# Kernel optimization log

Measured on AMD Instinct MI355X. Metric: run time of the kernel, lower is better.

The kernel has to match this reference:

```python
import jax, jax.numpy as jnp
import numpy as np
from jax import lax

C = 8          # bargs.channel
S = 1024       # bargs.test_sidelen
SIGMA = 1.0    # edge_sigma
KS = int(6 * SIGMA + 1)   # 7
PAD = KS // 2             # 3
BW = S // 6               # border_width
LAM, MU, TH = 5.0, 5.0, 1e-4


def _edge_kernel():
    coords = jnp.arange(KS, dtype=jnp.float32) - (KS - 1.0) / 2.0
    g1 = jnp.exp(-coords ** 2 / (2.0 * SIGMA ** 2))
    g1 = g1 / g1.sum()
    g2 = jnp.outer(g1, g1)
    return jnp.broadcast_to(g2, (C, 1, KS, KS))  # depthwise OIHW


def _alpha():
    # max applicable loop index among {row-dist, col-dist}; interior stays 1.
    r = jnp.arange(S)
    g = jnp.where(r < BW, r, jnp.where(S - 1 - r < BW, S - 1 - r, -1))  # [S]
    m = jnp.maximum(g[:, None], g[None, :])                              # [S,S]
    a = jnp.where(m >= 0, m.astype(jnp.float32) / BW, 1.0)
    return a[None, None]  # [1,1,S,S] broadcasts over channels


def _grad_spectrum():
    gv = jnp.array([[-1., -2., -1.], [0., 0., 0.], [1., 2., 1.]], jnp.float32)
    gh = gv.T
    gvf = jnp.fft.fft2(gv, s=(S, S))
    ghf = jnp.fft.fft2(gh, s=(S, S))
    return (jnp.abs(gvf) ** 2 + jnp.abs(ghf) ** 2).astype(jnp.float32)  # real


def _edge_blur(img, kernel, alpha):
    blurred = lax.conv_general_dilated(
        img, kernel, window_strides=(1, 1), padding=[(PAD, PAD), (PAD, PAD)],
        feature_group_count=C, dimension_numbers=('NCHW', 'OIHW', 'NCHW'))
    return alpha * img + (1.0 - alpha) * blurred


def setup_inputs() -> dict:
    key = jax.random.key(0)
    k1, k2 = jax.random.split(key)
    lms = jax.random.uniform(k1, (1, C, S, S), dtype=jnp.float32)
    fuse = jax.random.uniform(k2, (1, C, S, S), dtype=jnp.float32)
    return {"lms": lms, "fuse": fuse}


def reference(lms, fuse):
    kernel = _edge_kernel()
    alpha = _alpha()
    grad = _grad_spectrum()

    lms_fft = jnp.fft.fft2(_edge_blur(lms, kernel, alpha))
    fuse_fft = jnp.fft.fft2(_edge_blur(fuse, kernel, alpha))

    denom = jnp.abs(fuse_fft) ** 2 + LAM + MU * grad      # real [1,C,S,S]
    numer = jnp.conj(fuse_fft) * lms_fft
    psf = jnp.fft.fftshift(jnp.real(jnp.fft.ifft2(numer / denom)), axes=(-2, -1))
    psf = jnp.where(psf < TH, 0.0, psf)                   # [1,C,S,S]

    def crop(p):  # p: [S,S]
        row, col = jnp.unravel_index(jnp.argmax(p), p.shape)
        patch = lax.dynamic_slice(p, (row - 20, col - 20), (41, 41))
        return patch / jnp.sum(patch)

    psf_l = jax.vmap(crop)(psf[0])        # [C,41,41]
    return psf_l[:, None]                 # [C,1,41,41]
```

## Files before the change

kernel.cpp:

```cpp
#include <hip/hip_runtime.h>
#include <math.h>

#define SS 1024
#define NC 8
#define BWD 170
#define THRESH 1e-4f

typedef unsigned long long ull;

__device__ __forceinline__ float2 cmul(float2 a, float2 b) {
    return make_float2(a.x * b.x - a.y * b.y, a.x * b.y + a.y * b.x);
}

template <int DIRSIGN>
__device__ __forceinline__ void fft_fill_lut(float2* lut, int tid) {
    for (int i = tid; i < 768; i += 256) {
        float ang = (float)DIRSIGN * 6.28318530717958647692f * (float)i *
                    (1.0f / 1024.0f);
        float sv, cv;
        sincosf(ang, &sv, &cv);
        lut[i] = make_float2(cv, sv);
    }
}

template <int DIRSIGN, bool CONJ>
__device__ __forceinline__ void fft_stages(float2* bufA, float2* bufB,
                                           const float2* lut, int tid) {
    float2* src = bufA;
    float2* dst = bufB;
    #pragma unroll
    for (int t = 0; t < 5; ++t) {
        int s = 1 << (2 * t);
        int k = tid & ~(s - 1);
        float2 a = src[tid];
        float2 b = src[tid + 256];
        float2 c = src[tid + 512];
        float2 d = src[tid + 768];
        float2 apc = make_float2(a.x + c.x, a.y + c.y);
        float2 amc = make_float2(a.x - c.x, a.y - c.y);
        float2 bpd = make_float2(b.x + d.x, b.y + d.y);
        float2 jb  = make_float2(-(b.y - d.y), b.x - d.x);
        float2 t1, t3;
        if (DIRSIGN == -1) {
            t1 = make_float2(amc.x - jb.x, amc.y - jb.y);
            t3 = make_float2(amc.x + jb.x, amc.y + jb.y);
        } else {
            t1 = make_float2(amc.x + jb.x, amc.y + jb.y);
            t3 = make_float2(amc.x - jb.x, amc.y - jb.y);
        }
        float2 w1 = lut[k], w2 = lut[2 * k], w3 = lut[3 * k];
        if (CONJ) { w1.y = -w1.y; w2.y = -w2.y; w3.y = -w3.y; }
        int base = tid + 3 * k;
        dst[base]         = make_float2(apc.x + bpd.x, apc.y + bpd.y);
        dst[base + s]     = cmul(t1, w1);
        dst[base + 2 * s] = cmul(make_float2(apc.x - bpd.x, apc.y - bpd.y), w2);
        dst[base + 3 * s] = cmul(t3, w3);
        __syncthreads();
        float2* tmp = src; src = dst; dst = tmp;
    }
}

#define PIDX(r) ((r) + ((r) >> 5))

__global__ __launch_bounds__(256) void blur_fft_kernel(
        const float* __restrict__ lms, const float* __restrict__ fuse,
        float2* __restrict__ Zf) {
    __shared__ float2 bufA[1024];
    __shared__ float smemB[2136];
    __shared__ float2 lut[768];
    float2* bufB = (float2*)smemB;
    float* rowl = smemB;
    float* rowf = smemB + 1068;
    int tid = threadIdx.x;
    int g = blockIdx.x;
    int c = g >> 10;
    int y = (g & 7) * 128 + ((g >> 3) & 127);
    const float* L = lms + ((size_t)c << 20);
    const float* F = fuse + ((size_t)c << 20);
    int x0 = tid << 2;

    double e1 = exp(-0.5), e2 = exp(-2.0), e3 = exp(-4.5);
    double sm = 1.0 + 2.0 * (e1 + e2 + e3);
    float w[7] = { (float)(e3 / sm), (float)(e2 / sm), (float)(e1 / sm),
                   (float)(1.0 / sm),
                   (float)(e1 / sm), (float)(e2 / sm), (float)(e3 / sm) };

    bool rowInt = (y >= BWD) && (y <= SS - 1 - BWD);
    bool skipLoads = rowInt && (tid >= 45) && (tid <= 210);
    bool doH = !rowInt || (tid <= 43) || (tid >= 212);

    float4 cl, cf;
    if (skipLoads) {
        cl = *(const float4*)&L[((size_t)y << 10) + x0];
        cf = *(const float4*)&F[((size_t)y << 10) + x0];
    } else {
        float4 lv[7], fv[7];
        #pragma unroll
        for (int r = 0; r < 7; ++r) {
            int gy = y - 3 + r;
            if (gy >= 0 && gy < SS) {
                lv[r] = *(const float4*)&L[((size_t)gy << 10) + x0];
                fv[r] = *(const float4*)&F[((size_t)gy << 10) + x0];
            } else {
                lv[r] = make_float4(0.f, 0.f, 0.f, 0.f);
                fv[r] = make_float4(0.f, 0.f, 0.f, 0.f);
            }
        }
        cl = lv[3]; cf = fv[3];
        #pragma unroll
        for (int j = 0; j < 4; ++j) {
            float a = 0.f, b = 0.f;
            #pragma unroll
            for (int r = 0; r < 7; ++r) {
                a += w[r] * (&lv[r].x)[j];
                b += w[r] * (&fv[r].x)[j];
            }
            rowl[PIDX(3 + x0 + j)] = a;
            rowf[PIDX(3 + x0 + j)] = b;
        }
    }
    if (tid < 3) {
        rowl[PIDX(tid)] = 0.f; rowf[PIDX(tid)] = 0.f;
        rowl[PIDX(1027 + tid)] = 0.f; rowf[PIDX(1027 + tid)] = 0.f;
    }
    fft_fill_lut<-1>(lut, tid);
    __syncthreads();

    float bl[4] = {0.f, 0.f, 0.f, 0.f}, bf[4] = {0.f, 0.f, 0.f, 0.f};
    if (doH) {
        #pragma unroll
        for (int k = 0; k < 4; ++k) {
            float a = 0.f, b = 0.f;
            #pragma unroll
            for (int j = 0; j < 7; ++j) {
                a += w[j] * rowl[PIDX(x0 + k + j)];
                b += w[j] * rowf[PIDX(x0 + k + j)];
            }
            bl[k] = a; bf[k] = b;
        }
    }
    int gyv = (y < BWD) ? y : ((SS - 1 - y) < BWD ? (SS - 1 - y) : -1);
    #pragma unroll
    for (int k = 0; k < 4; ++k) {
        int x = x0 + k;
        int gx = (x < BWD) ? x : ((SS - 1 - x) < BWD ? (SS - 1 - x) : -1);
        int m = gyv > gx ? gyv : gx;
        float a = (m >= 0) ? (float)m / (float)BWD : 1.0f;
        bufA[x] = make_float2(a * (&cl.x)[k] + (1.0f - a) * bl[k],
                              a * (&cf.x)[k] + (1.0f - a) * bf[k]);
    }
    __syncthreads();
    fft_stages<-1, false>(bufA, bufB, lut, tid);
    float4* go = (float4*)(Zf + (((size_t)c << 20) + ((size_t)y << 10)));
    #pragma unroll
    for (int h = 0; h < 2; ++h) {
        int k = (tid + (h << 8)) << 1;
        float2 v0 = bufB[k], v1 = bufB[k + 1];
        go[tid + (h << 8)] = make_float4(v0.x, v0.y, v1.x, v1.y);
    }
}

__global__ __launch_bounds__(256) void fft2_wiener_kernel(
        const float2* __restrict__ Z, float2* __restrict__ Wb) {
    __shared__ float2 resbuf[4][1024];
    __shared__ float2 scratch[1024];
    __shared__ float2 lut[768];
    int tid = threadIdx.x;
    int p = blockIdx.x >> 9;
    int i = blockIdx.x & 511;
    int rows[2];
    rows[0] = (i == 0) ? 0 : i;
    rows[1] = (i == 0) ? 512 : 1024 - i;
    bool selfp = (i == 0);

    fft_fill_lut<-1>(lut, tid);

    const float4* g = (const float4*)(Z + (((size_t)(2 * p) << 20) +
                                           ((size_t)rows[0] << 10)));
    float4 ra = g[tid], rb = g[tid + 256];
    #pragma unroll
    for (int combo = 0; combo < 4; ++combo) {
        int k0 = tid << 1, k1 = (tid + 256) << 1;
        scratch[k0]     = make_float2(ra.x, ra.y);
        scratch[k0 + 1] = make_float2(ra.z, ra.w);
        scratch[k1]     = make_float2(rb.x, rb.y);
        scratch[k1 + 1] = make_float2(rb.z, rb.w);
        if (combo < 3) {
            int nr = (combo + 1) >> 1, nc = (combo + 1) & 1;
            const float4* gn = (const float4*)(Z +
                (((size_t)(2 * p + nc) << 20) + ((size_t)rows[nr] << 10)));
            ra = gn[tid];
            rb = gn[tid + 256];
        }
        __syncthreads();
        fft_stages<-1, false>(scratch, resbuf[combo], lut, tid);
    }

    const float TPN = 6.28318530717958647692f / 1024.0f;
    float2 gout[2][4];
    #pragma unroll
    for (int o = 0; o < 2; ++o) {
        int u = rows[o];
        int po = selfp ? o : (1 - o);
        float cu = cosf(TPN * (float)u);
        float c2u = 2.0f * cu * cu - 1.0f;
        float hu = 2.0f + 2.0f * cu;
        #pragma unroll
        for (int j = 0; j < 4; ++j) {
            int v = tid + (j << 8);
            int vn = (1024 - v) & 1023;
            float cv = cosf(TPN * (float)v);
            float c2v = 2.0f * cv * cv - 1.0f;
            float hv = 2.0f + 2.0f * cv;
            float grad = (2.0f - 2.0f * c2v) * hu * hu +
                         (2.0f - 2.0f * c2u) * hv * hv;
            float regs = 5.0f + 5.0f * grad;
            float G0x, G0y, G1x, G1y;
            #pragma unroll
            for (int c = 0; c < 2; ++c) {
                float2 a = resbuf[o * 2 + c][v];
                float2 b = resbuf[po * 2 + c][vn];
                float Lx = 0.5f * (a.x + b.x), Ly = 0.5f * (a.y - b.y);
                float Fx = 0.5f * (a.y + b.y), Fy = -0.5f * (a.x - b.x);
                float inv = 1.0f / (Fx * Fx + Fy * Fy + regs);
                float nx = (Fx * Lx + Fy * Ly) * inv;
                float ny = (Fx * Ly - Fy * Lx) * inv;
                if (c == 0) { G0x = nx; G0y = ny; } else { G1x = nx; G1y = ny; }
            }
            gout[o][j] = make_float2(G0x - G1y, G0y + G1x);
        }
    }
    __syncthreads();

    const float isc = 1.0f / 1024.0f;
    #pragma unroll
    for (int o = 0; o < 2; ++o) {
        #pragma unroll
        for (int j = 0; j < 4; ++j) scratch[tid + (j << 8)] = gout[o][j];
        __syncthreads();
        fft_stages<1, true>(scratch, resbuf[o], lut, tid);
        float4* go = (float4*)(Wb + (((size_t)p << 20) +
                                     ((size_t)rows[o] << 10)));
        #pragma unroll
        for (int h = 0; h < 2; ++h) {
            int k = (tid + (h << 8)) << 1;
            float2 v0 = resbuf[o][k], v1 = resbuf[o][k + 1];
            go[tid + (h << 8)] = make_float4(v0.x * isc, v0.y * isc,
                                             v1.x * isc, v1.y * isc);
        }
    }
}

__global__ __launch_bounds__(256) void ifft_final_kernel(
        const float2* __restrict__ Wd, float* __restrict__ psf,
        ull* __restrict__ bm) {
    __shared__ float2 bufA[1024];
    __shared__ float2 bufB[1024];
    __shared__ float2 lut[768];
    __shared__ ull red[256];
    int tid = threadIdx.x;
    size_t base = (size_t)blockIdx.x << 10;
    const float4* g = (const float4*)(Wd + base);
    #pragma unroll
    for (int h = 0; h < 2; ++h) {
        float4 v = g[tid + (h << 8)];
        int k = (tid + (h << 8)) << 1;
        bufA[k]     = make_float2(v.x, v.y);
        bufA[k + 1] = make_float2(v.z, v.w);
    }
    fft_fill_lut<1>(lut, tid);
    __syncthreads();
    fft_stages<1, false>(bufA, bufB, lut, tid);
    int p = blockIdx.x >> 10;
    int y = blockIdx.x & 1023;
    int oy = (y + 512) & 1023;
    float* p0 = psf + (((size_t)(2 * p) << 20) + ((size_t)oy << 10));
    float* p1 = p0 + (1u << 20);
    const float sc = 1.0f / 1024.0f;
    ull e0 = 0, e1 = 0;
    for (int k = tid; k < 1024; k += 256) {
        float2 v = bufB[k];
        float re = v.x * sc; re = (re < THRESH) ? 0.0f : re;
        float im = v.y * sc; im = (im < THRESH) ? 0.0f : im;
        int ox = (k + 512) & 1023;
        p0[ox] = re;
        p1[ox] = im;
        unsigned int idx = ((unsigned int)oy << 10) | (unsigned int)ox;
        ull c0 = ((ull)__float_as_uint(re) << 32) | (ull)(0xFFFFFFFFu - idx);
        ull c1 = ((ull)__float_as_uint(im) << 32) | (ull)(0xFFFFFFFFu - idx);
        e0 = c0 > e0 ? c0 : e0;
        e1 = c1 > e1 ? c1 : e1;
    }
    red[tid] = e0;
    __syncthreads();
    for (int s2 = 128; s2 > 0; s2 >>= 1) {
        if (tid < s2) { ull a = red[tid], b = red[tid + s2]; red[tid] = a > b ? a : b; }
        __syncthreads();
    }
    if (tid == 0) bm[((size_t)(2 * p) << 10) + y] = red[0];
    __syncthreads();
    red[tid] = e1;
    __syncthreads();
    for (int s2 = 128; s2 > 0; s2 >>= 1) {
        if (tid < s2) { ull a = red[tid], b = red[tid + s2]; red[tid] = a > b ? a : b; }
        __syncthreads();
    }
    if (tid == 0) bm[((size_t)(2 * p + 1) << 10) + y] = red[0];
}

__global__ __launch_bounds__(256) void transpose_kernel(float2* __restrict__ A) {
    __shared__ float2 ta[32][33];
    __shared__ float2 tb[32][33];
    float2* P = A + ((size_t)blockIdx.y << 20);
    int r = blockIdx.x, bi = 0;
    while (r >= 32 - bi) { r -= 32 - bi; ++bi; }
    int bj = bi + r;
    int tx = threadIdx.x & 31, ty = threadIdx.x >> 5;
    for (int yy = ty; yy < 32; yy += 8) {
        ta[yy][tx] = P[(size_t)(bi * 32 + yy) * SS + bj * 32 + tx];
        tb[yy][tx] = P[(size_t)(bj * 32 + yy) * SS + bi * 32 + tx];
    }
    __syncthreads();
    for (int yy = ty; yy < 32; yy += 8) {
        P[(size_t)(bi * 32 + yy) * SS + bj * 32 + tx] = tb[tx][yy];
        P[(size_t)(bj * 32 + yy) * SS + bi * 32 + tx] = ta[tx][yy];
    }
}

__global__ __launch_bounds__(256) void crop_kernel(
        const float* __restrict__ psf, const ull* __restrict__ bm,
        float* __restrict__ out) {
    int c = blockIdx.x;
    __shared__ ull rmax[256];
    __shared__ float red[256];
    int tid = threadIdx.x;
    ull e = 0;
    for (int i = tid; i < 1024; i += 256) {
        ull v = bm[((size_t)c << 10) + i];
        e = v > e ? v : e;
    }
    rmax[tid] = e;
    __syncthreads();
    for (int s2 = 128; s2 > 0; s2 >>= 1) {
        if (tid < s2) { ull a = rmax[tid], b = rmax[tid + s2]; rmax[tid] = a > b ? a : b; }
        __syncthreads();
    }
    unsigned int bidx = 0xFFFFFFFFu - (unsigned int)(rmax[0] & 0xFFFFFFFFull);
    int row = (int)(bidx >> 10), col = (int)(bidx & 1023);
    int r0 = row - 20; if (r0 < 0) r0 = 0; if (r0 > SS - 41) r0 = SS - 41;
    int c0 = col - 20; if (c0 < 0) c0 = 0; if (c0 > SS - 41) c0 = SS - 41;
    const float* p = psf + ((size_t)c << 20);
    float local = 0.0f;
    for (int i = tid; i < 1681; i += 256) {
        int rr = i / 41, cc = i - rr * 41;
        local += p[(size_t)(r0 + rr) * SS + c0 + cc];
    }
    red[tid] = local;
    __syncthreads();
    for (int s2 = 128; s2 > 0; s2 >>= 1) {
        if (tid < s2) red[tid] += red[tid + s2];
        __syncthreads();
    }
    float inv = 1.0f / red[0];
    for (int i = tid; i < 1681; i += 256) {
        int rr = i / 41, cc = i - rr * 41;
        out[c * 1681 + i] = p[(size_t)(r0 + rr) * SS + c0 + cc] * inv;
    }
}

extern "C" void kernel_launch(void* const* d_in, const int* in_sizes, int n_in,
                              void* d_out, int out_size, void* d_ws,
                              size_t ws_size, hipStream_t stream) {
    const float* lms = (const float*)d_in[0];
    const float* fuse = (const float*)d_in[1];
    char* ws = (char*)d_ws;
    float2* Zf = (float2*)ws;
    float2* Wb = (float2*)(ws + ((size_t)64 << 20));
    float* psf = (float*)ws;
    ull* bm = (ull*)(ws + ((size_t)33 << 20));
    float* outp = (float*)d_out;

    blur_fft_kernel<<<8192, 256, 0, stream>>>(lms, fuse, Zf);
    transpose_kernel<<<dim3(528, 8), 256, 0, stream>>>(Zf);
    fft2_wiener_kernel<<<2048, 256, 0, stream>>>(Zf, Wb);
    transpose_kernel<<<dim3(528, 4), 256, 0, stream>>>(Wb);
    ifft_final_kernel<<<4096, 256, 0, stream>>>(Wb, psf, bm);
    crop_kernel<<<8, 256, 0, stream>>>(psf, bm, outp);
}
```

Measured before the change: 232.4 us.

## Keep radix-4 FFT data in registers with XOR-swizzled LDS exchanges

Rewrites the 1024-point Stockham FFT so each thread keeps its four points in registers. Data goes through shared memory only between stages, and the last butterfly runs in registers, so results are written straight to global memory in natural order. Shared-memory indices are XOR-swizzled to cut bank conflicts. Twiddle and gradient-spectrum trig now use the hardware sin/cos intrinsics on revolution inputs. This removes LDS round trips and staging copies, at the cost of more register pressure and slightly lower trig accuracy.

```diff
diff --git a/kernel.cpp b/kernel.cpp
--- a/kernel.cpp
+++ b/kernel.cpp
@@ -12,52 +12,64 @@
     return make_float2(a.x * b.x - a.y * b.y, a.x * b.y + a.y * b.x);
 }
 
+#define XS(a) ((a) ^ (((a) >> 4) & 15))
+
 template <int DIRSIGN>
 __device__ __forceinline__ void fft_fill_lut(float2* lut, int tid) {
     for (int i = tid; i < 768; i += 256) {
-        float ang = (float)DIRSIGN * 6.28318530717958647692f * (float)i *
-                    (1.0f / 1024.0f);
-        float sv, cv;
-        sincosf(ang, &sv, &cv);
-        lut[i] = make_float2(cv, sv);
+        float rev = (float)i * (1.0f / 1024.0f);
+        float cv = __builtin_amdgcn_cosf(rev);
+        float sv = __builtin_amdgcn_sinf(rev);
+        lut[i] = make_float2(cv, (float)DIRSIGN * sv);
+    }
+}
+
+template <int DIRSIGN>
+__device__ __forceinline__ void bfly4(const float2 v[4], float2 r[4]) {
+    float2 a = v[0], b = v[1], c = v[2], d = v[3];
+    float2 apc = make_float2(a.x + c.x, a.y + c.y);
+    float2 amc = make_float2(a.x - c.x, a.y - c.y);
+    float2 bpd = make_float2(b.x + d.x, b.y + d.y);
+    float2 jb  = make_float2(-(b.y - d.y), b.x - d.x);
+    r[0] = make_float2(apc.x + bpd.x, apc.y + bpd.y);
+    r[2] = make_float2(apc.x - bpd.x, apc.y - bpd.y);
+    if (DIRSIGN == -1) {
+        r[1] = make_float2(amc.x - jb.x, amc.y - jb.y);
+        r[3] = make_float2(amc.x + jb.x, amc.y + jb.y);
+    } else {
+        r[1] = make_float2(amc.x + jb.x, amc.y + jb.y);
+        r[3] = make_float2(amc.x - jb.x, amc.y - jb.y);
     }
 }
 
 template <int DIRSIGN, bool CONJ>
-__device__ __forceinline__ void fft_stages(float2* bufA, float2* bufB,
-                                           const float2* lut, int tid) {
-    float2* src = bufA;
-    float2* dst = bufB;
-    #pragma unroll
-    for (int t = 0; t < 5; ++t) {
+__device__ __forceinline__ void fft1024_reg(float2 v[4], float2* A, float2* B,
+                                            const float2* lut, int tid) {
+    float2* dst = A;
+    float2* alt = B;
+    #pragma unroll
+    for (int t = 0; t < 4; ++t) {
         int s = 1 << (2 * t);
         int k = tid & ~(s - 1);
-        float2 a = src[tid];
-        float2 b = src[tid + 256];
-        float2 c = src[tid + 512];
-        float2 d = src[tid + 768];
-        float2 apc = make_float2(a.x + c.x, a.y + c.y);
-        float2 amc = make_float2(a.x - c.x, a.y - c.y);
-        float2 bpd = make_float2(b.x + d.x, b.y + d.y);
-        float2 jb  = make_float2(-(b.y - d.y), b.x - d.x);
-        float2 t1, t3;
-        if (DIRSIGN == -1) {
-            t1 = make_float2(amc.x - jb.x, amc.y - jb.y);
-            t3 = make_float2(amc.x + jb.x, amc.y + jb.y);
-        } else {
-            t1 = make_float2(amc.x + jb.x, amc.y + jb.y);
-            t3 = make_float2(amc.x - jb.x, amc.y - jb.y);
-        }
+        float2 r[4];
+        bfly4<DIRSIGN>(v, r);
         float2 w1 = lut[k], w2 = lut[2 * k], w3 = lut[3 * k];
         if (CONJ) { w1.y = -w1.y; w2.y = -w2.y; w3.y = -w3.y; }
         int base = tid + 3 * k;
-        dst[base]         = make_float2(apc.x + bpd.x, apc.y + bpd.y);
-        dst[base + s]     = cmul(t1, w1);
-        dst[base + 2 * s] = cmul(make_float2(apc.x - bpd.x, apc.y - bpd.y), w2);
-        dst[base + 3 * s] = cmul(t3, w3);
-        __syncthreads();
-        float2* tmp = src; src = dst; dst = tmp;
-    }
+        dst[XS(base)]         = r[0];
+        dst[XS(base + s)]     = cmul(r[1], w1);
+        dst[XS(base + 2 * s)] = cmul(r[2], w2);
+        dst[XS(base + 3 * s)] = cmul(r[3], w3);
+        __syncthreads();
+        v[0] = dst[XS(tid)];
+        v[1] = dst[XS(tid + 256)];
+        v[2] = dst[XS(tid + 512)];
+        v[3] = dst[XS(tid + 768)];
+        float2* tmp = dst; dst = alt; alt = tmp;
+    }
+    float2 r[4];
+    bfly4<DIRSIGN>(v, r);
+    v[0] = r[0]; v[1] = r[1]; v[2] = r[2]; v[3] = r[3];
 }
 
 #define PIDX(r) ((r) + ((r) >> 5))
@@ -66,11 +78,10 @@
         const float* __restrict__ lms, const float* __restrict__ fuse,
         float2* __restrict__ Zf) {
     __shared__ float2 bufA[1024];
-    __shared__ float smemB[2136];
+    __shared__ float2 smemB2[1068];
     __shared__ float2 lut[768];
-    float2* bufB = (float2*)smemB;
-    float* rowl = smemB;
-    float* rowf = smemB + 1068;
+    float* rowl = (float*)smemB2;
+    float* rowf = rowl + 1068;
     int tid = threadIdx.x;
     int g = blockIdx.x;
     int c = g >> 10;
@@ -146,18 +157,19 @@
         int gx = (x < BWD) ? x : ((SS - 1 - x) < BWD ? (SS - 1 - x) : -1);
         int m = gyv > gx ? gyv : gx;
         float a = (m >= 0) ? (float)m / (float)BWD : 1.0f;
-        bufA[x] = make_float2(a * (&cl.x)[k] + (1.0f - a) * bl[k],
-                              a * (&cf.x)[k] + (1.0f - a) * bf[k]);
-    }
-    __syncthreads();
-    fft_stages<-1, false>(bufA, bufB, lut, tid);
-    float4* go = (float4*)(Zf + (((size_t)c << 20) + ((size_t)y << 10)));
-    #pragma unroll
-    for (int h = 0; h < 2; ++h) {
-        int k = (tid + (h << 8)) << 1;
-        float2 v0 = bufB[k], v1 = bufB[k + 1];
-        go[tid + (h << 8)] = make_float4(v0.x, v0.y, v1.x, v1.y);
-    }
+        bufA[XS(x)] = make_float2(a * (&cl.x)[k] + (1.0f - a) * bl[k],
+                                  a * (&cf.x)[k] + (1.0f - a) * bf[k]);
+    }
+    __syncthreads();
+
+    float2 v[4];
+    #pragma unroll
+    for (int m = 0; m < 4; ++m) v[m] = bufA[XS(tid + (m << 8))];
+    fft1024_reg<-1, false>(v, smemB2, bufA, lut, tid);
+
+    float2* Zrow = Zf + (((size_t)c << 20) + ((size_t)y << 10));
+    #pragma unroll
+    for (int r = 0; r < 4; ++r) Zrow[tid + (r << 8)] = v[r];
 }
 
 __global__ __launch_bounds__(256) void fft2_wiener_kernel(
@@ -174,42 +186,48 @@
     bool selfp = (i == 0);
 
     fft_fill_lut<-1>(lut, tid);
-
-    const float4* g = (const float4*)(Z + (((size_t)(2 * p) << 20) +
-                                           ((size_t)rows[0] << 10)));
-    float4 ra = g[tid], rb = g[tid + 256];
+    __syncthreads();
+
+    float2 v[4], nv[4];
+    {
+        const float2* g0 = Z + (((size_t)(2 * p) << 20) +
+                                ((size_t)rows[0] << 10));
+        #pragma unroll
+        for (int m = 0; m < 4; ++m) v[m] = g0[tid + (m << 8)];
+    }
     #pragma unroll
     for (int combo = 0; combo < 4; ++combo) {
-        int k0 = tid << 1, k1 = (tid + 256) << 1;
-        scratch[k0]     = make_float2(ra.x, ra.y);
-        scratch[k0 + 1] = make_float2(ra.z, ra.w);
-        scratch[k1]     = make_float2(rb.x, rb.y);
-        scratch[k1 + 1] = make_float2(rb.z, rb.w);
         if (combo < 3) {
             int nr = (combo + 1) >> 1, nc = (combo + 1) & 1;
-            const float4* gn = (const float4*)(Z +
-                (((size_t)(2 * p + nc) << 20) + ((size_t)rows[nr] << 10)));
-            ra = gn[tid];
-            rb = gn[tid + 256];
-        }
-        __syncthreads();
-        fft_stages<-1, false>(scratch, resbuf[combo], lut, tid);
-    }
-
-    const float TPN = 6.28318530717958647692f / 1024.0f;
+            const float2* gn = Z + (((size_t)(2 * p + nc) << 20) +
+                                    ((size_t)rows[nr] << 10));
+            #pragma unroll
+            for (int m = 0; m < 4; ++m) nv[m] = gn[tid + (m << 8)];
+        }
+        fft1024_reg<-1, false>(v, scratch, resbuf[combo], lut, tid);
+        #pragma unroll
+        for (int r = 0; r < 4; ++r)
+            resbuf[combo][XS(tid + (r << 8))] = v[r];
+        if (combo < 3) {
+            #pragma unroll
+            for (int m = 0; m < 4; ++m) v[m] = nv[m];
+        }
+    }
+    __syncthreads();
+
     float2 gout[2][4];
     #pragma unroll
     for (int o = 0; o < 2; ++o) {
         int u = rows[o];
         int po = selfp ? o : (1 - o);
-        float cu = cosf(TPN * (float)u);
+        float cu = __builtin_amdgcn_cosf((float)u * (1.0f / 1024.0f));
         float c2u = 2.0f * cu * cu - 1.0f;
         float hu = 2.0f + 2.0f * cu;
         #pragma unroll
         for (int j = 0; j < 4; ++j) {
-            int v = tid + (j << 8);
-            int vn = (1024 - v) & 1023;
-            float cv = cosf(TPN * (float)v);
+            int vv = tid + (j << 8);
+            int vn = (1024 - vv) & 1023;
+            float cv = __builtin_amdgcn_cosf((float)vv * (1.0f / 1024.0f));
             float c2v = 2.0f * cv * cv - 1.0f;
             float hv = 2.0f + 2.0f * cv;
             float grad = (2.0f - 2.0f * c2v) * hu * hu +
@@ -218,8 +236,8 @@
             float G0x, G0y, G1x, G1y;
             #pragma unroll
             for (int c = 0; c < 2; ++c) {
-                float2 a = resbuf[o * 2 + c][v];
-                float2 b = resbuf[po * 2 + c][vn];
+                float2 a = resbuf[o * 2 + c][XS(vv)];
+                float2 b = resbuf[po * 2 + c][XS(vn)];
                 float Lx = 0.5f * (a.x + b.x), Ly = 0.5f * (a.y - b.y);
                 float Fx = 0.5f * (a.y + b.y), Fy = -0.5f * (a.x - b.x);
                 float inv = 1.0f / (Fx * Fx + Fy * Fy + regs);
@@ -235,19 +253,14 @@
     const float isc = 1.0f / 1024.0f;
     #pragma unroll
     for (int o = 0; o < 2; ++o) {
-        #pragma unroll
-        for (int j = 0; j < 4; ++j) scratch[tid + (j << 8)] = gout[o][j];
-        __syncthreads();
-        fft_stages<1, true>(scratch, resbuf[o], lut, tid);
-        float4* go = (float4*)(Wb + (((size_t)p << 20) +
-                                     ((size_t)rows[o] << 10)));
-        #pragma unroll
-        for (int h = 0; h < 2; ++h) {
-            int k = (tid + (h << 8)) << 1;
-            float2 v0 = resbuf[o][k], v1 = resbuf[o][k + 1];
-            go[tid + (h << 8)] = make_float4(v0.x * isc, v0.y * isc,
-                                             v1.x * isc, v1.y * isc);
-        }
+        float2 iv[4];
+        #pragma unroll
+        for (int j = 0; j < 4; ++j) iv[j] = gout[o][j];
+        fft1024_reg<1, true>(iv, scratch, resbuf[o], lut, tid);
+        float2* go = Wb + (((size_t)p << 20) + ((size_t)rows[o] << 10));
+        #pragma unroll
+        for (int r = 0; r < 4; ++r)
+            go[tid + (r << 8)] = make_float2(iv[r].x * isc, iv[r].y * isc);
     }
 }
 
@@ -259,18 +272,14 @@
     __shared__ float2 lut[768];
     __shared__ ull red[256];
     int tid = threadIdx.x;
-    size_t base = (size_t)blockIdx.x << 10;
-    const float4* g = (const float4*)(Wd + base);
-    #pragma unroll
-    for (int h = 0; h < 2; ++h) {
-        float4 v = g[tid + (h << 8)];
-        int k = (tid + (h << 8)) << 1;
-        bufA[k]     = make_float2(v.x, v.y);
-        bufA[k + 1] = make_float2(v.z, v.w);
-    }
+    const float2* g = Wd + ((size_t)blockIdx.x << 10);
+    float2 v[4];
+    #pragma unroll
+    for (int m = 0; m < 4; ++m) v[m] = g[tid + (m << 8)];
     fft_fill_lut<1>(lut, tid);
     __syncthreads();
-    fft_stages<1, false>(bufA, bufB, lut, tid);
+    fft1024_reg<1, false>(v, bufA, bufB, lut, tid);
+
     int p = blockIdx.x >> 10;
     int y = blockIdx.x & 1023;
     int oy = (y + 512) & 1023;
@@ -278,10 +287,11 @@
     float* p1 = p0 + (1u << 20);
     const float sc = 1.0f / 1024.0f;
     ull e0 = 0, e1 = 0;
-    for (int k = tid; k < 1024; k += 256) {
-        float2 v = bufB[k];
-        float re = v.x * sc; re = (re < THRESH) ? 0.0f : re;
-        float im = v.y * sc; im = (im < THRESH) ? 0.0f : im;
+    #pragma unroll
+    for (int r = 0; r < 4; ++r) {
+        int k = tid + (r << 8);
+        float re = v[r].x * sc; re = (re < THRESH) ? 0.0f : re;
+        float im = v[r].y * sc; im = (im < THRESH) ? 0.0f : im;
         int ox = (k + 512) & 1023;
         p0[ox] = re;
         p1[ox] = im;
```

Measured after the change: 215.1 us. 1.08x faster.
